# Kernel tuning notes

Hardware: AMD Instinct MI355X
Metric: run time of the kernel (lower is better)

The kernel has to match this reference:

```python
import jax, jax.numpy as jnp
import numpy as np
from jax import lax

S = 8192      # total tokens
HID = 1280    # hidden_size
H = 16        # num_heads
D = HID // H  # head_dim = 80
NSEG = 8      # number of equal-length segments (images)


def rotate_half(x):
    half = x.shape[-1] // 2
    return jnp.concatenate([-x[..., half:], x[..., :half]], axis=-1)


def setup_inputs() -> dict:
    key = jax.random.key(0)
    k1, k2, k3, k4 = jax.random.split(key, 4)
    hidden_states = jax.random.normal(k1, (S, HID), dtype=jnp.float32)
    # rotary embeddings: angles repeated over both halves, as in standard vision RoPE
    theta = jax.random.uniform(k2, (S, D // 2), dtype=jnp.float32) * (2.0 * np.pi)
    freqs = jnp.concatenate([theta, theta], axis=-1)  # [S, D]
    cos = jnp.cos(freqs)
    sin = jnp.sin(freqs)
    qkv_kernel = jax.random.normal(k3, (HID, 3, H, D), dtype=jnp.float32) * 0.02
    qkv_bias = jnp.zeros((3, H, D), dtype=jnp.float32)
    proj_kernel = jax.random.normal(k4, (H * D, HID), dtype=jnp.float32) * 0.02
    proj_bias = jnp.zeros((HID,), dtype=jnp.float32)
    cu_seqlens = jnp.arange(NSEG + 1, dtype=jnp.int32) * (S // NSEG)
    return {
        "hidden_states": hidden_states, "cos": cos, "sin": sin,
        "qkv_kernel": qkv_kernel, "qkv_bias": qkv_bias,
        "proj_kernel": proj_kernel, "proj_bias": proj_bias,
        "cu_seqlens": cu_seqlens,
    }


def reference(hidden_states, cos, sin, qkv_kernel, qkv_bias, proj_kernel, proj_bias, cu_seqlens):
    P = lax.Precision.HIGHEST
    seq, dtype = hidden_states.shape[0], hidden_states.dtype
    # fused QKV projection: [S, 3, H, D]
    qkv = jnp.einsum('sd,dtnh->stnh', hidden_states, qkv_kernel, precision=P) + qkv_bias
    q, k, v = qkv[:, 0], qkv[:, 1], qkv[:, 2]
    # rotary position embedding in fp32 (as in original)
    cf = cos[:, None, :].astype(jnp.float32)
    sf = sin[:, None, :].astype(jnp.float32)
    qf = q.astype(jnp.float32)
    kf = k.astype(jnp.float32)
    q = (qf * cf + rotate_half(qf) * sf).astype(dtype)
    k = (kf * cf + rotate_half(kf) * sf).astype(dtype)
    # block-diagonal attention over equal-length segments from cu_seqlens
    n_seg = cu_seqlens.shape[0] - 1
    L = seq // n_seg  # segment length (uniform segments)
    head_dim = q.shape[-1]
    scale = head_dim ** (-0.5)
    qs = q.reshape(n_seg, L, H, head_dim)
    ks = k.reshape(n_seg, L, H, head_dim)
    vs = v.reshape(n_seg, L, H, head_dim)
    logits = jnp.einsum('bqhd,bkhd->bhqk', qs, ks, precision=P) * scale
    attn = jax.nn.softmax(logits.astype(jnp.float32), axis=-1).astype(dtype)
    out = jnp.einsum('bhqk,bkhd->bqhd', attn, vs, precision=P).reshape(seq, H * head_dim)
    return jnp.einsum('se,ed->sd', out, proj_kernel, precision=P) + proj_bias
```

## Files before the change

### kernel.cpp

```cpp
#include <hip/hip_runtime.h>

#define S_LEN 8192
#define HID   1280
#define NHEAD 16
#define HD    80
#define NQKV  3840
#define VTS   8256

#define GLOBAL_AS __attribute__((address_space(1)))
#define LDS_AS    __attribute__((address_space(3)))

typedef __attribute__((ext_vector_type(8))) short bf16x8;
typedef __attribute__((ext_vector_type(4))) float f32x4;
typedef __attribute__((ext_vector_type(4))) unsigned short u16x4;
typedef __attribute__((ext_vector_type(8))) unsigned short u16x8;
typedef __attribute__((ext_vector_type(2))) unsigned int u32x2;

__device__ __forceinline__ unsigned short f2bf(float f) {
    union { float f; unsigned int u; } v; v.f = f;
    unsigned int r = v.u + 0x7FFFu + ((v.u >> 16) & 1u);
    return (unsigned short)(r >> 16);
}
__device__ __forceinline__ float bf2f(unsigned short h) {
    union { unsigned int u; float f; } v; v.u = ((unsigned int)h) << 16;
    return v.f;
}
__device__ __forceinline__ unsigned int cvt_pk_bf16(float a, float b) {
    unsigned int r;
    asm("v_cvt_pk_bf16_f32 %0, %1, %2" : "=v"(r) : "v"(a), "v"(b));
    return r;
}

__global__ __launch_bounds__(256) void k_cvt(const float* __restrict__ src,
                                             unsigned short* __restrict__ dst, int n4)
{
    int i = blockIdx.x * 256 + threadIdx.x;
    if (i >= n4) return;
    f32x4 v = *(const f32x4*)&src[(size_t)i * 4];
    u16x4 o;
    o[0] = f2bf(v[0]); o[1] = f2bf(v[1]); o[2] = f2bf(v[2]); o[3] = f2bf(v[3]);
    *(u16x4*)&dst[(size_t)i * 4] = o;
}

__global__ __launch_bounds__(256) void k_wt(const float* __restrict__ W,
                                            unsigned short* __restrict__ Wt,
                                            int R, int C)
{
    __shared__ float T[32][33];
    int r0 = blockIdx.y * 32, c0 = blockIdx.x * 32;
    int tr = threadIdx.x >> 3, tc = (threadIdx.x & 7) * 4;
    f32x4 v = *(const f32x4*)&W[(size_t)(r0 + tr) * C + c0 + tc];
    T[tr][tc + 0] = v[0]; T[tr][tc + 1] = v[1];
    T[tr][tc + 2] = v[2]; T[tr][tc + 3] = v[3];
    __syncthreads();
    int c = threadIdx.x >> 3, r4 = (threadIdx.x & 7) * 4;
    u16x4 o;
    o[0] = f2bf(T[r4 + 0][c]); o[1] = f2bf(T[r4 + 1][c]);
    o[2] = f2bf(T[r4 + 2][c]); o[3] = f2bf(T[r4 + 3][c]);
    *(u16x4*)&Wt[(size_t)(c0 + c) * R + r0 + r4] = o;
}

__global__ __launch_bounds__(256) void k_vtr(const unsigned short* __restrict__ vb,
                                             unsigned short* __restrict__ vt)
{
    const int b = blockIdx.x;
    const int h = b >> 6, s0 = (b & 63) * 128;
    const int tid = threadIdx.x;
    if (tid >= 160) return;
    const int sblk = tid & 15, dch = tid >> 4;
    u16x8 a[8];
#pragma unroll
    for (int j = 0; j < 8; ++j)
        a[j] = *(const u16x8*)&vb[(size_t)(s0 + sblk * 8 + j) * HID + h * HD + dch * 8];
#pragma unroll
    for (int jj = 0; jj < 8; ++jj) {
        u16x8 o;
#pragma unroll
        for (int j = 0; j < 8; ++j) o[j] = a[j][jj];
        *(u16x8*)&vt[(size_t)(h * HD + dch * 8 + jj) * VTS + s0 + sblk * 8] = o;
    }
}

template<int MODE>
__global__ __launch_bounds__(512, 2) void k_gemm256(
    const unsigned short* __restrict__ A,
    const unsigned short* __restrict__ Bt,
    const float* __restrict__ bias,
    unsigned short* __restrict__ q0, unsigned short* __restrict__ k0p,
    unsigned short* __restrict__ v0, float* __restrict__ fo)
{
    __shared__ __align__(16) unsigned short As[2][2][16][64][8];
    __shared__ __align__(16) unsigned short Bs[2][2][16][64][8];
    const int tid = threadIdx.x;
    const int w = tid >> 6, l = tid & 63;
    const int qg = l & 15, g = l >> 4;
    const int wm = w >> 2, wn = w & 3;
    const int wm8 = wm * 8, wn4 = wn * 4;

    const int bid = blockIdx.x;
    const int xcd = bid & 7, t = bid >> 3;
    const int bm0 = (xcd * 4 + (t & 3)) * 256;
    const int bn0 = (t >> 2) * 256;

    const unsigned short* ga = A + (size_t)(bm0 + w * 16 + qg) * HID + g * 8;
    const unsigned short* gb = Bt + (size_t)(bn0 + w * 16 + qg) * HID + g * 8;

#define SG_A(d, ks, kcol) do {                                                  \
    __builtin_amdgcn_global_load_lds((const GLOBAL_AS unsigned int*)(ga + (kcol)), \
        (LDS_AS unsigned int*)&As[d][ks][w][0][0], 16, 0, 0);                   \
    __builtin_amdgcn_global_load_lds((const GLOBAL_AS unsigned int*)(ga + (size_t)128 * HID + (kcol)), \
        (LDS_AS unsigned int*)&As[d][ks][8 + w][0][0], 16, 0, 0); } while (0)
#define SG_B(d, ks, kcol) do {                                                  \
    __builtin_amdgcn_global_load_lds((const GLOBAL_AS unsigned int*)(gb + (kcol)), \
        (LDS_AS unsigned int*)&Bs[d][ks][w][0][0], 16, 0, 0);                   \
    __builtin_amdgcn_global_load_lds((const GLOBAL_AS unsigned int*)(gb + (size_t)128 * HID + (kcol)), \
        (LDS_AS unsigned int*)&Bs[d][ks][8 + w][0][0], 16, 0, 0); } while (0)

#define RD_A4(d, ks, fb) do {                                                   \
    af[0] = *(const bf16x8*)&As[d][ks][wm8 + (fb) + 0][l][0];                   \
    af[1] = *(const bf16x8*)&As[d][ks][wm8 + (fb) + 1][l][0];                   \
    af[2] = *(const bf16x8*)&As[d][ks][wm8 + (fb) + 2][l][0];                   \
    af[3] = *(const bf16x8*)&As[d][ks][wm8 + (fb) + 3][l][0]; } while (0)
#define RD_B4(d, ks) do {                                                       \
    bf[0] = *(const bf16x8*)&Bs[d][ks][wn4 + 0][l][0];                          \
    bf[1] = *(const bf16x8*)&Bs[d][ks][wn4 + 1][l][0];                          \
    bf[2] = *(const bf16x8*)&Bs[d][ks][wn4 + 2][l][0];                          \
    bf[3] = *(const bf16x8*)&Bs[d][ks][wn4 + 3][l][0]; } while (0)

#define MFMAQ(base) do {                                                        \
    _Pragma("unroll")                                                           \
    for (int m = 0; m < 4; ++m)                                                 \
        _Pragma("unroll")                                                       \
        for (int n = 0; n < 4; ++n)                                             \
            acc[(base) + m][n] = __builtin_amdgcn_mfma_f32_16x16x32_bf16(       \
                af[m], bf[n], acc[(base) + m][n], 0, 0, 0); } while (0)

#define BARW() do { __builtin_amdgcn_s_barrier();                               \
    asm volatile("s_waitcnt lgkmcnt(0)" ::: "memory");                          \
    __builtin_amdgcn_sched_barrier(0);                                          \
    __builtin_amdgcn_s_setprio(1); } while (0)
#define BARC() do { __builtin_amdgcn_s_setprio(0);                              \
    __builtin_amdgcn_s_barrier();                                               \
    __builtin_amdgcn_sched_barrier(0); } while (0)
#define BARC_VM4() do { __builtin_amdgcn_s_setprio(0);                          \
    asm volatile("s_waitcnt vmcnt(4)" ::: "memory");                            \
    __builtin_amdgcn_s_barrier();                                               \
    __builtin_amdgcn_sched_barrier(0); } while (0)
#define BARC_VM0() do { __builtin_amdgcn_s_setprio(0);                          \
    asm volatile("s_waitcnt vmcnt(0)" ::: "memory");                            \
    __builtin_amdgcn_s_barrier();                                               \
    __builtin_amdgcn_sched_barrier(0); } while (0)

    f32x4 acc[8][4];
#pragma unroll
    for (int m = 0; m < 8; ++m)
#pragma unroll
        for (int n = 0; n < 4; ++n) acc[m][n] = (f32x4){0.f, 0.f, 0.f, 0.f};

    SG_A(0, 0, 0);  SG_B(0, 0, 0);
    SG_A(0, 1, 32); SG_B(0, 1, 32);
    SG_A(1, 0, 64); SG_B(1, 0, 64);
    asm volatile("s_waitcnt vmcnt(4)" ::: "memory");
    __builtin_amdgcn_s_barrier();
    __builtin_amdgcn_sched_barrier(0);

    const int NIT = HID / 128;
    for (int j = 0; j < NIT; ++j) {
        const bool st = (j + 1 < NIT);
        const int c1 = j * 128 + 96;
        const int c2 = j * 128 + 128;
        const int c2b = j * 128 + 160;
        const int c3 = j * 128 + 192;
        bf16x8 af[4], bf[4];

        RD_A4(0, 0, 0); RD_B4(0, 0);
        SG_A(1, 1, c1);
        BARW(); MFMAQ(0); BARC();
        RD_A4(0, 0, 4);
        SG_B(1, 1, c1);
        BARW(); MFMAQ(4); BARC();
        RD_A4(0, 1, 0); RD_B4(0, 1);
        if (st) SG_A(0, 0, c2);
        BARW(); MFMAQ(0); BARC();
        RD_A4(0, 1, 4);
        if (st) SG_B(0, 0, c2);
        BARW(); MFMAQ(4);
        if (st) BARC_VM4(); else BARC_VM0();
        RD_A4(1, 0, 0); RD_B4(1, 0);
        if (st) SG_A(0, 1, c2b);
        BARW(); MFMAQ(0); BARC();
        RD_A4(1, 0, 4);
        if (st) SG_B(0, 1, c2b);
        BARW(); MFMAQ(4); BARC();
        RD_A4(1, 1, 0); RD_B4(1, 1);
        if (st) SG_A(1, 0, c3);
        BARW(); MFMAQ(0); BARC();
        RD_A4(1, 1, 4);
        if (st) SG_B(1, 0, c3);
        BARW(); MFMAQ(4);
        if (st) BARC_VM4(); else BARC_VM0();
    }
#undef SG_A
#undef SG_B
#undef RD_A4
#undef RD_B4
#undef MFMAQ
#undef BARW
#undef BARC
#undef BARC_VM4
#undef BARC_VM0

    if constexpr (MODE == 0) {
        const int t3 = bn0 / HID;
        unsigned short* dst = (t3 == 0) ? q0 : ((t3 == 1) ? k0p : v0);
        const int colbase = bn0 - t3 * HID + wn * 64;
#pragma unroll
        for (int n = 0; n < 4; ++n) {
            const int col = colbase + n * 16 + qg;
            const float bv = bias[bn0 + wn * 64 + n * 16 + qg];
#pragma unroll
            for (int m = 0; m < 8; ++m)
#pragma unroll
                for (int r = 0; r < 4; ++r) {
                    const int row = bm0 + wm * 128 + m * 16 + g * 4 + r;
                    dst[(size_t)row * HID + col] = f2bf(acc[m][n][r] + bv);
                }
        }
    } else {
#pragma unroll
        for (int n = 0; n < 4; ++n) {
            const int col = bn0 + wn * 64 + n * 16 + qg;
            const float bv = bias[col];
#pragma unroll
            for (int m = 0; m < 8; ++m)
#pragma unroll
                for (int r = 0; r < 4; ++r) {
                    const int row = bm0 + wm * 128 + m * 16 + g * 4 + r;
                    fo[(size_t)row * HID + col] = acc[m][n][r] + bv;
                }
        }
    }
}

__global__ __launch_bounds__(256) void k_rope(
    unsigned short* __restrict__ qb, unsigned short* __restrict__ kb,
    const float* __restrict__ cosb, const float* __restrict__ sinb)
{
    const float SCQ = 0.11180339887498949f * 1.44269504088896340f;
    int idx = blockIdx.x * 256 + threadIdx.x;
    if (idx >= S_LEN * NHEAD * 10) return;
    int s = idx / 160;
    int rem = idx - s * 160;
    int nh = rem / 10, h4 = (rem - nh * 10) * 4;
    size_t base = (size_t)s * HID + nh * HD + h4;
    f32x4 c0 = *(const f32x4*)&cosb[s * HD + h4];
    f32x4 c1 = *(const f32x4*)&cosb[s * HD + h4 + 40];
    f32x4 s0 = *(const f32x4*)&sinb[s * HD + h4];
    f32x4 s1 = *(const f32x4*)&sinb[s * HD + h4 + 40];
    u16x4 qa = *(const u16x4*)&qb[base];
    u16x4 qb4 = *(const u16x4*)&qb[base + 40];
    u16x4 ka = *(const u16x4*)&kb[base];
    u16x4 kb4 = *(const u16x4*)&kb[base + 40];
    u16x4 o0, o1, p0, p1;
#pragma unroll
    for (int j = 0; j < 4; ++j) {
        float qaf = bf2f(qa[j]), qbf = bf2f(qb4[j]);
        o0[j] = f2bf((qaf * c0[j] - qbf * s0[j]) * SCQ);
        o1[j] = f2bf((qbf * c1[j] + qaf * s1[j]) * SCQ);
        float kaf = bf2f(ka[j]), kbf = bf2f(kb4[j]);
        p0[j] = f2bf(kaf * c0[j] - kbf * s0[j]);
        p1[j] = f2bf(kbf * c1[j] + kaf * s1[j]);
    }
    *(u16x4*)&qb[base] = o0;
    *(u16x4*)&qb[base + 40] = o1;
    *(u16x4*)&kb[base] = p0;
    *(u16x4*)&kb[base + 40] = p1;
}

__global__ __launch_bounds__(256) void k_attn(
    const unsigned short* __restrict__ qb, const unsigned short* __restrict__ kbuf,
    const unsigned short* __restrict__ vt, unsigned short* __restrict__ ao)
{
    __shared__ __align__(16) unsigned short Ks[2][64][104];
    __shared__ __align__(16) unsigned short Vs[2][80][64];
    __shared__ __align__(16) unsigned short Pls[4][2][16][68];

    const int tid = threadIdx.x;
    const int w = tid >> 6, l = tid & 63;
    const int qg = l & 15, g = l >> 4;
    const int wb = w << 6;
    const int vxor = (qg & 7) << 4;

    const int b = blockIdx.x;
    const int xcd = b & 7, j = b >> 3;
    const int p = xcd * 16 + (j >> 3);
    const int qt = j & 7;
    const int seg = p >> 4, head = p & 15;
    const int row0 = seg * 1024 + qt * 128 + w * 32;
    const size_t hoff = (size_t)head * HD;
    const int vhead = head * HD;
    const int kb0 = seg * 1024;

#define STAGE(bi, kr0_)                                                        \
    {                                                                          \
        const int kr0s = (kr0_);                                               \
        _Pragma("unroll")                                                      \
        for (int i = 0; i < 4; ++i) {                                          \
            const int u = i * 256 + tid;                                       \
            if (u < 832) {                                                     \
                const int r = u / 13, cu = (u - r * 13) * 8;                   \
                __builtin_amdgcn_global_load_lds(                              \
                    (const GLOBAL_AS unsigned int*)&kbuf[(size_t)(kr0s + r) * HID + hoff + cu], \
                    (LDS_AS unsigned int*)((LDS_AS unsigned short*)&Ks[bi][0][0] + (size_t)(i * 256 + wb) * 8), \
                    16, 0, 0);                                                 \
            }                                                                  \
        }                                                                      \
        _Pragma("unroll")                                                      \
        for (int i = 0; i < 3; ++i) {                                          \
            const int u = i * 256 + tid;                                       \
            if (u < 640) {                                                     \
                const int r = u >> 3;                                          \
                const int cs = ((u & 7) * 16) ^ ((r & 7) << 4);                \
                __builtin_amdgcn_global_load_lds(                              \
                    (const GLOBAL_AS unsigned int*)&vt[(size_t)(vhead + r) * VTS + kr0s + (cs >> 1)], \
                    (LDS_AS unsigned int*)((LDS_AS unsigned short*)&Vs[bi][0][0] + (size_t)(i * 256 + wb) * 8), \
                    16, 0, 0);                                                 \
            }                                                                  \
        }                                                                      \
    }

#define COMPUTE(bi)                                                            \
    {                                                                          \
        f32x4 st[2][4];                                                        \
        _Pragma("unroll")                                                      \
        for (int s = 0; s < 2; ++s)                                            \
            _Pragma("unroll")                                                  \
            for (int kn = 0; kn < 4; ++kn) st[s][kn] = (f32x4){0.f, 0.f, 0.f, 0.f}; \
        _Pragma("unroll")                                                      \
        for (int ks = 0; ks < 3; ++ks)                                         \
            _Pragma("unroll")                                                  \
            for (int kn = 0; kn < 4; ++kn) {                                   \
                bf16x8 kf = *(const bf16x8*)&Ks[bi][kn * 16 + qg][ks * 32 + g * 8]; \
                st[0][kn] = __builtin_amdgcn_mfma_f32_16x16x32_bf16(kf, qf[0][ks], st[0][kn], 0, 0, 0); \
                st[1][kn] = __builtin_amdgcn_mfma_f32_16x16x32_bf16(kf, qf[1][ks], st[1][kn], 0, 0, 0); \
            }                                                                  \
        _Pragma("unroll")                                                      \
        for (int s = 0; s < 2; ++s) {                                          \
            float psum = 0.f;                                                  \
            _Pragma("unroll")                                                  \
            for (int kn = 0; kn < 4; ++kn) {                                   \
                float p0 = exp2f(st[s][kn][0]);                                \
                float p1 = exp2f(st[s][kn][1]);                                \
                float p2 = exp2f(st[s][kn][2]);                                \
                float p3 = exp2f(st[s][kn][3]);                                \
                psum += (p0 + p1) + (p2 + p3);                                 \
                u32x2 pk;                                                      \
                pk[0] = cvt_pk_bf16(p0, p1);                                   \
                pk[1] = cvt_pk_bf16(p2, p3);                                   \
                *(u32x2*)&Pls[w][s][qg][kn * 16 + g * 4] = pk;                 \
            }                                                                  \
            psum += __shfl_xor(psum, 16, 64);                                  \
            psum += __shfl_xor(psum, 32, 64);                                  \
            lsum[s] += psum;                                                   \
        }                                                                      \
        _Pragma("unroll")                                                      \
        for (int ks = 0; ks < 2; ++ks) {                                       \
            bf16x8 pf0 = *(const bf16x8*)&Pls[w][0][qg][ks * 32 + g * 8];      \
            bf16x8 pf1 = *(const bf16x8*)&Pls[w][1][qg][ks * 32 + g * 8];      \
            _Pragma("unroll")                                                  \
            for (int d = 0; d < 5; ++d) {                                      \
                bf16x8 vf = *(const bf16x8*)((const unsigned short*)&Vs[bi][0][0] + \
                    (d * 16 + qg) * 64 + (((ks * 64 + g * 16) ^ vxor) >> 1));  \
                acc[0][d] = __builtin_amdgcn_mfma_f32_16x16x32_bf16(vf, pf0, acc[0][d], 0, 0, 0); \
                acc[1][d] = __builtin_amdgcn_mfma_f32_16x16x32_bf16(vf, pf1, acc[1][d], 0, 0, 0); \
            }                                                                  \
        }                                                                      \
    }

    bf16x8 qf[2][3];
#pragma unroll
    for (int s = 0; s < 2; ++s)
#pragma unroll
        for (int ks = 0; ks < 3; ++ks) {
            if (ks < 2 || g < 2)
                qf[s][ks] = *(const bf16x8*)&qb[(size_t)(row0 + s * 16 + qg) * HID + hoff + ks * 32 + g * 8];
            else
                qf[s][ks] = (bf16x8)(short)0;
        }

    float lsum[2] = {0.f, 0.f};
    f32x4 acc[2][5];
#pragma unroll
    for (int s = 0; s < 2; ++s)
#pragma unroll
        for (int d = 0; d < 5; ++d) acc[s][d] = (f32x4){0.f, 0.f, 0.f, 0.f};

    STAGE(0, kb0);
    __syncthreads();
    for (int ch = 0; ch < 16; ch += 2) {
        if (ch + 1 < 16) STAGE(1, kb0 + (ch + 1) * 64);
        COMPUTE(0);
        __syncthreads();
        if (ch + 2 < 16) STAGE(0, kb0 + (ch + 2) * 64);
        COMPUTE(1);
        __syncthreads();
    }

#pragma unroll
    for (int s = 0; s < 2; ++s) {
        const float inv = 1.0f / lsum[s];
        const int orow = row0 + s * 16 + qg;
#pragma unroll
        for (int d = 0; d < 5; ++d) {
            u16x4 o;
#pragma unroll
            for (int r = 0; r < 4; ++r) o[r] = f2bf(acc[s][d][r] * inv);
            *(u16x4*)&ao[(size_t)orow * HID + hoff + d * 16 + g * 4] = o;
        }
    }
#undef STAGE
#undef COMPUTE
}

extern "C" void kernel_launch(void* const* d_in, const int* in_sizes, int n_in,
                              void* d_out, int out_size, void* d_ws, size_t ws_size,
                              hipStream_t stream)
{
    (void)in_sizes; (void)n_in; (void)out_size; (void)ws_size;
    const float* hidden = (const float*)d_in[0];
    const float* cosb   = (const float*)d_in[1];
    const float* sinb   = (const float*)d_in[2];
    const float* qkv_w  = (const float*)d_in[3];
    const float* qkv_b  = (const float*)d_in[4];
    const float* proj_w = (const float*)d_in[5];
    const float* proj_b = (const float*)d_in[6];

    float* out = (float*)d_out;
    unsigned short* ws = (unsigned short*)d_ws;
    const size_t n = (size_t)S_LEN * HID;
    unsigned short* hb     = ws;
    unsigned short* wqkvt  = hb + n;
    unsigned short* wprojt = wqkvt + (size_t)NQKV * HID;
    unsigned short* qb     = wprojt + (size_t)HID * HID;
    unsigned short* kb     = qb + n;
    unsigned short* vb     = kb + n;
    unsigned short* vt     = vb + n;
    unsigned short* aob    = vt + (size_t)NHEAD * HD * VTS;

    k_cvt<<<(int)((n / 4 + 255) / 256), 256, 0, stream>>>(hidden, hb, (int)(n / 4));
    dim3 gw1(NQKV / 32, HID / 32);
    k_wt<<<gw1, 256, 0, stream>>>(qkv_w, wqkvt, HID, NQKV);
    dim3 gw2(HID / 32, HID / 32);
    k_wt<<<gw2, 256, 0, stream>>>(proj_w, wprojt, HID, HID);

    k_gemm256<0><<<480, 512, 0, stream>>>(hb, wqkvt, qkv_b, qb, kb, vb, nullptr);

    k_rope<<<(S_LEN * NHEAD * 10 + 255) / 256, 256, 0, stream>>>(qb, kb, cosb, sinb);

    k_vtr<<<NHEAD * (S_LEN / 128), 256, 0, stream>>>(vb, vt);

    k_attn<<<1024, 256, 0, stream>>>(qb, kb, vt, aob);

    k_gemm256<1><<<160, 512, 0, stream>>>(aob, wprojt, proj_b, nullptr, nullptr, nullptr, out);
}
```

Baseline: 279.3 us.

## Replace output projection GEMM with smaller-tile kernel for better CU occupancy

The output projection GEMM used 256x256 tiles, which gave only 160 blocks on a 256-CU device. A new k_proj kernel uses 128x128 tiles with 256 threads, launching 640 blocks. It is a simple single-buffered loop with global_load_lds and MFMA 16x16x32. The QKV kernel is de-templated and its epilogue loop is reordered so bias values are hoisted. The new kernel gives up the double-buffered pipelining of the large-tile kernel in exchange for better CU fill.

Measured after the change: 257.2 us. 7.9% less time.

```diff
diff --git a/kernel.cpp b/kernel.cpp
--- a/kernel.cpp
+++ b/kernel.cpp
@@ -81,13 +81,12 @@
     }
 }
 
-template<int MODE>
-__global__ __launch_bounds__(512, 2) void k_gemm256(
+__global__ __launch_bounds__(512, 2) void k_qkv256(
     const unsigned short* __restrict__ A,
     const unsigned short* __restrict__ Bt,
     const float* __restrict__ bias,
     unsigned short* __restrict__ q0, unsigned short* __restrict__ k0p,
-    unsigned short* __restrict__ v0, float* __restrict__ fo)
+    unsigned short* __restrict__ v0)
 {
     __shared__ __align__(16) unsigned short As[2][2][16][64][8];
     __shared__ __align__(16) unsigned short Bs[2][2][16][64][8];
@@ -210,36 +209,22 @@
 #undef BARC_VM4
 #undef BARC_VM0
 
-    if constexpr (MODE == 0) {
-        const int t3 = bn0 / HID;
-        unsigned short* dst = (t3 == 0) ? q0 : ((t3 == 1) ? k0p : v0);
-        const int colbase = bn0 - t3 * HID + wn * 64;
-#pragma unroll
-        for (int n = 0; n < 4; ++n) {
-            const int col = colbase + n * 16 + qg;
-            const float bv = bias[bn0 + wn * 64 + n * 16 + qg];
-#pragma unroll
-            for (int m = 0; m < 8; ++m)
-#pragma unroll
-                for (int r = 0; r < 4; ++r) {
-                    const int row = bm0 + wm * 128 + m * 16 + g * 4 + r;
-                    dst[(size_t)row * HID + col] = f2bf(acc[m][n][r] + bv);
-                }
+    const int t3 = bn0 / HID;
+    unsigned short* dst = (t3 == 0) ? q0 : ((t3 == 1) ? k0p : v0);
+    const int colbase = bn0 - t3 * HID + wn * 64 + qg;
+    float bv[4];
+#pragma unroll
+    for (int n = 0; n < 4; ++n) bv[n] = bias[bn0 + wn * 64 + n * 16 + qg];
+#pragma unroll
+    for (int m = 0; m < 8; ++m)
+#pragma unroll
+        for (int r = 0; r < 4; ++r) {
+            const int row = bm0 + wm * 128 + m * 16 + g * 4 + r;
+            unsigned short* drow = dst + (size_t)row * HID + colbase;
+#pragma unroll
+            for (int n = 0; n < 4; ++n)
+                drow[n * 16] = f2bf(acc[m][n][r] + bv[n]);
         }
-    } else {
-#pragma unroll
-        for (int n = 0; n < 4; ++n) {
-            const int col = bn0 + wn * 64 + n * 16 + qg;
-            const float bv = bias[col];
-#pragma unroll
-            for (int m = 0; m < 8; ++m)
-#pragma unroll
-                for (int r = 0; r < 4; ++r) {
-                    const int row = bm0 + wm * 128 + m * 16 + g * 4 + r;
-                    fo[(size_t)row * HID + col] = acc[m][n][r] + bv;
-                }
-        }
-    }
 }
 
 __global__ __launch_bounds__(256) void k_rope(
@@ -422,6 +407,69 @@
 #undef COMPUTE
 }
 
+__global__ __launch_bounds__(256) void k_proj(
+    const unsigned short* __restrict__ A,
+    const unsigned short* __restrict__ Bt,
+    const float* __restrict__ bias, float* __restrict__ out)
+{
+    __shared__ __align__(16) unsigned short As[128][32];
+    __shared__ __align__(16) unsigned short Bs[128][32];
+    const int tid = threadIdx.x;
+    const int w = tid >> 6, l = tid & 63;
+    const int qg = l & 15, g = l >> 4;
+    const int wr = w >> 1, wc = w & 1;
+    const int bid = blockIdx.x;
+    const int xcd = bid & 7, t = bid >> 3;
+    const int bm0 = (xcd * 8 + (t & 7)) * 128;
+    const int bn0 = (t >> 3) * 128;
+
+    f32x4 acc[4][4];
+#pragma unroll
+    for (int m = 0; m < 4; ++m)
+#pragma unroll
+        for (int n = 0; n < 4; ++n) acc[m][n] = (f32x4){0.f, 0.f, 0.f, 0.f};
+
+    const int lr = l >> 2, lc = (l & 3) * 8;
+    const unsigned short* ga = A + (size_t)(bm0 + w * 16 + lr) * HID + lc;
+    const unsigned short* gb = Bt + (size_t)(bn0 + w * 16 + lr) * HID + lc;
+    LDS_AS unsigned int* la0 = (LDS_AS unsigned int*)&As[w * 16][0];
+    LDS_AS unsigned int* la1 = (LDS_AS unsigned int*)&As[w * 16 + 64][0];
+    LDS_AS unsigned int* lb0 = (LDS_AS unsigned int*)&Bs[w * 16][0];
+    LDS_AS unsigned int* lb1 = (LDS_AS unsigned int*)&Bs[w * 16 + 64][0];
+
+    for (int k0 = 0; k0 < HID; k0 += 32) {
+        __syncthreads();
+        __builtin_amdgcn_global_load_lds((const GLOBAL_AS unsigned int*)(ga + k0), la0, 16, 0, 0);
+        __builtin_amdgcn_global_load_lds((const GLOBAL_AS unsigned int*)(ga + (size_t)64 * HID + k0), la1, 16, 0, 0);
+        __builtin_amdgcn_global_load_lds((const GLOBAL_AS unsigned int*)(gb + k0), lb0, 16, 0, 0);
+        __builtin_amdgcn_global_load_lds((const GLOBAL_AS unsigned int*)(gb + (size_t)64 * HID + k0), lb1, 16, 0, 0);
+        __syncthreads();
+        bf16x8 af[4], bff[4];
+#pragma unroll
+        for (int m = 0; m < 4; ++m) af[m] = *(const bf16x8*)&As[wr * 64 + m * 16 + qg][g * 8];
+#pragma unroll
+        for (int n = 0; n < 4; ++n) bff[n] = *(const bf16x8*)&Bs[wc * 64 + n * 16 + qg][g * 8];
+#pragma unroll
+        for (int m = 0; m < 4; ++m)
+#pragma unroll
+            for (int n = 0; n < 4; ++n)
+                acc[m][n] = __builtin_amdgcn_mfma_f32_16x16x32_bf16(af[m], bff[n], acc[m][n], 0, 0, 0);
+    }
+
+#pragma unroll
+    for (int n = 0; n < 4; ++n) {
+        const int col = bn0 + wc * 64 + n * 16 + qg;
+        const float bv = bias[col];
+#pragma unroll
+        for (int m = 0; m < 4; ++m)
+#pragma unroll
+            for (int r = 0; r < 4; ++r) {
+                const int row = bm0 + wr * 64 + m * 16 + g * 4 + r;
+                out[(size_t)row * HID + col] = acc[m][n][r] + bv;
+            }
+    }
+}
+
 extern "C" void kernel_launch(void* const* d_in, const int* in_sizes, int n_in,
                               void* d_out, int out_size, void* d_ws, size_t ws_size,
                               hipStream_t stream)
@@ -453,7 +501,7 @@
     dim3 gw2(HID / 32, HID / 32);
     k_wt<<<gw2, 256, 0, stream>>>(proj_w, wprojt, HID, HID);
 
-    k_gemm256<0><<<480, 512, 0, stream>>>(hb, wqkvt, qkv_b, qb, kb, vb, nullptr);
+    k_qkv256<<<480, 512, 0, stream>>>(hb, wqkvt, qkv_b, qb, kb, vb);
 
     k_rope<<<(S_LEN * NHEAD * 10 + 255) / 256, 256, 0, stream>>>(qb, kb, cosb, sinb);
 
@@ -461,5 +509,5 @@
 
     k_attn<<<1024, 256, 0, stream>>>(qb, kb, vt, aob);
 
-    k_gemm256<1><<<160, 512, 0, stream>>>(aob, wprojt, proj_b, nullptr, nullptr, nullptr, out);
-}
+    k_proj<<<640, 256, 0, stream>>>(aob, wprojt, proj_b, out);
+}
```
